# Performance work log

Hardware: AMD Instinct MI355X
Metric: run time of the kernel (lower is better)

Reference implementation:

```python
import jax, jax.numpy as jnp
import numpy as np

N_NODES = 50000
N_EDGES = 800000
D_IN = 128
D_HID = 512
D_OUT = 128


def setup_inputs() -> dict:
    key = jax.random.key(0)
    k1, k2, k3, k4, k5, k6 = jax.random.split(key, 6)
    input_matrix = jax.random.normal(k1, (N_NODES, D_IN), dtype=jnp.float32)
    adjacency_coo_matrix = jax.random.randint(k2, (2, N_EDGES), 0, N_NODES, dtype=jnp.int64)
    # fc net params (torch Linear: y = x @ W.T + b); store W already transposed [D_IN, D_HID]
    lim_fc = 1.0 / np.sqrt(D_IN)
    fc_w = jax.random.uniform(k3, (D_IN, D_HID), dtype=jnp.float32, minval=-lim_fc, maxval=lim_fc)
    fc_b = jax.random.uniform(k4, (D_HID,), dtype=jnp.float32, minval=-lim_fc, maxval=lim_fc)
    # xavier_uniform for [D_IN + D_HID, D_OUT]
    lim_w = np.sqrt(6.0 / (D_IN + D_HID + D_OUT))
    weights_matrix = jax.random.uniform(k5, (D_IN + D_HID, D_OUT), dtype=jnp.float32, minval=-lim_w, maxval=lim_w)
    return {
        "input_matrix": input_matrix,
        "fc_w": fc_w,
        "fc_b": fc_b,
        "weights_matrix": weights_matrix,
        "adjacency_coo_matrix": adjacency_coo_matrix,
    }


def reference(input_matrix, fc_w, fc_b, weights_matrix, adjacency_coo_matrix):
    edge_src, edge_trg = adjacency_coo_matrix[0], adjacency_coo_matrix[1]
    n_nodes = input_matrix.shape[0]
    # gather neighbor features: [E, D_IN]
    neighbors = input_matrix[edge_trg]
    # per-edge MLP + relu: [E, D_HID]
    neighbors_repr = jax.nn.relu(neighbors @ fc_w + fc_b)
    # scatter-max reduce into per-node slots; relu outputs are >= 0, and
    # empty segments map to 0 (matching torch_scatter zero-fill), so clamp at 0
    agg = jax.ops.segment_max(neighbors_repr, edge_src, num_segments=n_nodes)
    agg = jnp.maximum(agg, 0.0)
    concat = jnp.concatenate([input_matrix, agg], axis=1)  # [N, D_IN + D_HID]
    return concat @ weights_matrix  # [N, D_OUT]
```

## Files before the change

kernel.cpp:

```cpp
#include <hip/hip_runtime.h>
#include <hip/hip_bf16.h>

#define N_NODES 50000
#define N_EDGES 800000
#define D_IN 128
#define D_HID 512
#define D_OUT 128
#define CAT_DIM 640
#define CAP 64

typedef __attribute__((ext_vector_type(8))) short short8;
typedef __attribute__((ext_vector_type(4))) float floatx4;

__device__ __forceinline__ unsigned short f2bf(float f) {
    unsigned u = __float_as_uint(f);
    unsigned r = u + 0x7fffu + ((u >> 16) & 1u);
    return (unsigned short)(r >> 16);
}

__device__ __forceinline__ void cvt8(const float* __restrict__ src, unsigned short* o) {
    float4 v0 = *(const float4*)src;
    float4 v1 = *(const float4*)(src + 4);
    o[0] = f2bf(v0.x); o[1] = f2bf(v0.y); o[2] = f2bf(v0.z); o[3] = f2bf(v0.w);
    o[4] = f2bf(v1.x); o[5] = f2bf(v1.y); o[6] = f2bf(v1.z); o[7] = f2bf(v1.w);
}


#define NBKT 98
#define BKT_SHIFT 9
#define CAPB 12288
#define P1_CHUNK 4096
#define P1_BLOCKS 196


#define A_FCW_BLOCKS 256
#define A_W2_BLOCKS  320
#define A_BLOCKS (P1_BLOCKS + A_FCW_BLOCKS + A_W2_BLOCKS)

__global__ __launch_bounds__(256)
void prep_sort_kernel(const float* __restrict__ fcW, const float* __restrict__ Wm,
                      const int* __restrict__ adj,
                      unsigned short* __restrict__ fcwT,
                      unsigned short* __restrict__ WT,
                      int* __restrict__ bucket_cnt, uint2* __restrict__ staging) {
    int b = blockIdx.x, tid = threadIdx.x;
    if (b < P1_BLOCKS) {
        __shared__ uint2 les[P1_CHUNK];
        __shared__ int cnt[NBKT];
        __shared__ int woff[NBKT];
        for (int i = tid; i < NBKT; i += 256) cnt[i] = 0;
        int v = adj[2 * (tid & 63) + 1];
        int s = (__ballot(v != 0) == 0ULL) ? 2 : 1;
        __syncthreads();
        int e0 = b * P1_CHUNK;
        int ne = N_EDGES - e0; if (ne > P1_CHUNK) ne = P1_CHUNK;
        for (int j = tid; j < ne; j += 256) {
            int e = e0 + j;
            int src, trg;
            if (s == 2) { src = adj[2 * (size_t)e]; trg = adj[2 * ((size_t)N_EDGES + e)]; }
            else        { src = adj[e];             trg = adj[N_EDGES + e]; }
            les[j] = make_uint2((unsigned)src, (unsigned)trg);
            atomicAdd(&cnt[src >> BKT_SHIFT], 1);
        }
        __syncthreads();
        for (int i = tid; i < NBKT; i += 256)
            woff[i] = atomicAdd(&bucket_cnt[i], cnt[i]);
        __syncthreads();
        for (int j = tid; j < ne; j += 256) {
            uint2 et = les[j];
            int bk = (int)(et.x >> BKT_SHIFT);
            int pos = atomicAdd(&woff[bk], 1);
            if (pos < CAPB) staging[(size_t)bk * CAPB + pos] = et;
        }
        return;
    }
    b -= P1_BLOCKS;
    if (b < A_FCW_BLOCKS) {
        int idx = b * 256 + tid;
        int k = idx >> 9;
        int n = idx & (D_HID - 1);
        fcwT[n * D_IN + k] = f2bf(fcW[idx]);
        return;
    }
    b -= A_FCW_BLOCKS;
    {
        int idx = b * 256 + tid;
        int k = idx >> 7;
        int n = idx & (D_OUT - 1);
        WT[n * CAT_DIM + k] = f2bf(Wm[idx]);
    }
}


#define GEMM_MT      782
#define GEMM1_TILES (GEMM_MT * 4)
#define GPAD 8
#define SM_BYTES ((64 + 128) * (64 + GPAD) * 2)

__global__ __launch_bounds__(256)
void mid_kernel(const int* __restrict__ bucket_cnt, const uint2* __restrict__ staging,
                int* __restrict__ deg, int* __restrict__ edge_list,
                const float* __restrict__ X,
                const unsigned short* __restrict__ fcwT,
                const float* __restrict__ fcb,
                unsigned short* __restrict__ F) {
    __shared__ char smem[SM_BYTES];
    int tid = threadIdx.x;
    if (blockIdx.x < NBKT) {
        int* ldeg = (int*)smem;
        int bk = blockIdx.x;
        for (int i = tid; i < 512; i += 256) ldeg[i] = 0;
        __syncthreads();
        int n = bucket_cnt[bk]; if (n > CAPB) n = CAPB;
        int base = bk << BKT_SHIFT;
        const uint2* st = staging + (size_t)bk * CAPB;
        for (int i = tid; i < n; i += 256) {
            uint2 et = st[i];
            int p = atomicAdd(&ldeg[(int)et.x - base], 1);
            if (p < CAP) edge_list[(size_t)et.x * CAP + p] = (int)et.y;
        }
        __syncthreads();
        for (int i = tid; i < 512; i += 256) {
            int src = base + i;
            if (src < N_NODES) deg[src] = ldeg[i];
        }
        return;
    }
    typedef unsigned short RowA[64 + GPAD];
    RowA* As = (RowA*)smem;
    RowA* Bs = (RowA*)(smem + 64 * (64 + GPAD) * 2);
    int lane = tid & 63, w = tid >> 6;
    int tile = blockIdx.x - NBKT;
    int bm = (tile >> 2) * 64, bn = (tile & 3) * 128;
    int wm = (w >> 1) * 32, wn = (w & 1) * 64;
    int q = lane >> 4, l16 = lane & 15;
    floatx4 acc[2][4] = {};
    int ra = tid >> 2;
    int ca = (tid & 3) * 8;
    int rb = tid >> 1;
    int cb = (tid & 1) * 8;

    for (int k0 = 0; k0 < D_IN; k0 += 64) {
        {
            int gr = bm + ra;
            #pragma unroll
            for (int p = 0; p < 2; ++p) {
                unsigned short o[8] = {0, 0, 0, 0, 0, 0, 0, 0};
                if (gr < N_NODES) cvt8(X + (size_t)gr * D_IN + k0 + ca + p * 32, o);
                *(uint4*)(&As[ra][ca + p * 32]) = *(const uint4*)o;
            }
        }
        {
            const unsigned short* bp = fcwT + (size_t)(bn + rb) * D_IN + k0 + cb;
            #pragma unroll
            for (int p = 0; p < 4; ++p)
                *(uint4*)(&Bs[rb][cb + p * 16]) = *(const uint4*)(bp + p * 16);
        }
        __syncthreads();
        #pragma unroll
        for (int ks = 0; ks < 2; ++ks) {
            short8 af[2], bf[4];
            #pragma unroll
            for (int mi = 0; mi < 2; ++mi)
                af[mi] = *(const short8*)(&As[wm + mi * 16 + l16][ks * 32 + q * 8]);
            #pragma unroll
            for (int ni = 0; ni < 4; ++ni)
                bf[ni] = *(const short8*)(&Bs[wn + ni * 16 + l16][ks * 32 + q * 8]);
            #pragma unroll
            for (int mi = 0; mi < 2; ++mi)
                #pragma unroll
                for (int ni = 0; ni < 4; ++ni)
                    acc[mi][ni] = __builtin_amdgcn_mfma_f32_16x16x32_bf16(af[mi], bf[ni], acc[mi][ni], 0, 0, 0);
        }
        __syncthreads();
    }

    #pragma unroll
    for (int mi = 0; mi < 2; ++mi)
        #pragma unroll
        for (int ni = 0; ni < 4; ++ni)
            #pragma unroll
            for (int r = 0; r < 4; ++r) {
                int row = bm + wm + mi * 16 + q * 4 + r;
                int col = bn + wn + ni * 16 + l16;
                if (row < N_NODES) {
                    float v = fmaxf(acc[mi][ni][r] + fcb[col], 0.0f);
                    F[(size_t)row * D_HID + col] = f2bf(v);
                }
            }
}


__device__ __forceinline__ void fmax_bf16x8(float* acc, const uint4& p) {
    const unsigned* a = (const unsigned*)&p;
    #pragma unroll
    for (int j = 0; j < 4; ++j) {
        unsigned u = a[j];
        acc[2 * j]     = fmaxf(acc[2 * j],     __uint_as_float(u << 16));
        acc[2 * j + 1] = fmaxf(acc[2 * j + 1], __uint_as_float(u & 0xffff0000u));
    }
}

__global__ __launch_bounds__(256)
void aggregate_kernel(const unsigned short* __restrict__ F,
                      const int* __restrict__ deg,
                      const int* __restrict__ edge_list,
                      unsigned short* __restrict__ agg) {
    int gw = (blockIdx.x * 256 + threadIdx.x) >> 6;
    if (gw >= N_NODES) return;
    int lane = threadIdx.x & 63;
    int d = deg[gw];
    d = d < CAP ? d : CAP;
    const int* el = edge_list + gw * CAP;
    float acc[8] = {0.f, 0.f, 0.f, 0.f, 0.f, 0.f, 0.f, 0.f};
    int i = 0;
    for (; i + 2 <= d; i += 2) {
        int t0 = el[i], t1 = el[i + 1];
        uint4 p0 = *(const uint4*)(F + (size_t)t0 * D_HID + lane * 8);
        uint4 p1 = *(const uint4*)(F + (size_t)t1 * D_HID + lane * 8);
        fmax_bf16x8(acc, p0);
        fmax_bf16x8(acc, p1);
    }
    if (i < d) {
        uint4 p0 = *(const uint4*)(F + (size_t)el[i] * D_HID + lane * 8);
        fmax_bf16x8(acc, p0);
    }
    unsigned out[4];
    #pragma unroll
    for (int j = 0; j < 4; ++j) {
        unsigned lo = __float_as_uint(acc[2 * j]) >> 16;
        unsigned hi = __float_as_uint(acc[2 * j + 1]) & 0xffff0000u;
        out[j] = lo | hi;
    }
    *(uint4*)(agg + (size_t)gw * D_HID + lane * 8) = *(uint4*)out;
}


__global__ __launch_bounds__(256)
void gemm2_kernel(const float* __restrict__ X,
                  const unsigned short* __restrict__ agg,
                  const unsigned short* __restrict__ WT,
                  float* __restrict__ out) {
    __shared__ unsigned short As[64][64 + GPAD];
    __shared__ unsigned short Bs[128][64 + GPAD];
    int tid = threadIdx.x;
    int lane = tid & 63, w = tid >> 6;
    int wm = (w >> 1) * 32, wn = (w & 1) * 64;
    int q = lane >> 4, l16 = lane & 15;
    int bm = blockIdx.x * 64;
    floatx4 acc[2][4] = {};
    int ra = tid >> 2;
    int ca = (tid & 3) * 8;
    int rb = tid >> 1;
    int cb = (tid & 1) * 8;

    for (int k0 = 0; k0 < CAT_DIM; k0 += 64) {
        {
            int gr = bm + ra;
            #pragma unroll
            for (int p = 0; p < 2; ++p) {
                int col = k0 + ca + p * 32;
                unsigned short o[8] = {0, 0, 0, 0, 0, 0, 0, 0};
                if (gr < N_NODES) {
                    if (col < D_IN) cvt8(X + (size_t)gr * D_IN + col, o);
                    else *(uint4*)o = *(const uint4*)(agg + (size_t)gr * D_HID + (col - D_IN));
                }
                *(uint4*)(&As[ra][ca + p * 32]) = *(const uint4*)o;
            }
        }
        {
            const unsigned short* bp = WT + (size_t)rb * CAT_DIM + k0 + cb;
            #pragma unroll
            for (int p = 0; p < 4; ++p)
                *(uint4*)(&Bs[rb][cb + p * 16]) = *(const uint4*)(bp + p * 16);
        }
        __syncthreads();
        #pragma unroll
        for (int ks = 0; ks < 2; ++ks) {
            short8 af[2], bf[4];
            #pragma unroll
            for (int mi = 0; mi < 2; ++mi)
                af[mi] = *(const short8*)(&As[wm + mi * 16 + l16][ks * 32 + q * 8]);
            #pragma unroll
            for (int ni = 0; ni < 4; ++ni)
                bf[ni] = *(const short8*)(&Bs[wn + ni * 16 + l16][ks * 32 + q * 8]);
            #pragma unroll
            for (int mi = 0; mi < 2; ++mi)
                #pragma unroll
                for (int ni = 0; ni < 4; ++ni)
                    acc[mi][ni] = __builtin_amdgcn_mfma_f32_16x16x32_bf16(af[mi], bf[ni], acc[mi][ni], 0, 0, 0);
        }
        __syncthreads();
    }

    #pragma unroll
    for (int mi = 0; mi < 2; ++mi)
        #pragma unroll
        for (int ni = 0; ni < 4; ++ni)
            #pragma unroll
            for (int r = 0; r < 4; ++r) {
                int row = bm + wm + mi * 16 + q * 4 + r;
                int col = wn + ni * 16 + l16;
                if (row < N_NODES)
                    out[(size_t)row * D_OUT + col] = acc[mi][ni][r];
            }
}


extern "C" void kernel_launch(void* const* d_in, const int* in_sizes, int n_in,
                              void* d_out, int out_size, void* d_ws, size_t ws_size,
                              hipStream_t stream) {
    const float* X    = (const float*)d_in[0];
    const float* fc_w = (const float*)d_in[1];
    const float* fc_b = (const float*)d_in[2];
    const float* Wm   = (const float*)d_in[3];
    const int*   adj  = (const int*)d_in[4];
    float* outp = (float*)d_out;

    char* ws = (char*)d_ws;
    size_t off = 0;
    auto alloc = [&](size_t bytes) -> void* {
        void* p = ws + off;
        off = (off + bytes + 255) & ~(size_t)255;
        return p;
    };
    unsigned short* agg    = (unsigned short*)alloc((size_t)N_NODES * D_HID * 2);
    unsigned short* F      = (unsigned short*)alloc((size_t)N_NODES * D_HID * 2);
    unsigned short* fcwT   = (unsigned short*)alloc((size_t)D_HID * D_IN * 2);
    unsigned short* WT     = (unsigned short*)alloc((size_t)D_OUT * CAT_DIM * 2);
    int* deg       = (int*)alloc((size_t)N_NODES * 4);
    int* edge_list = (int*)alloc((size_t)N_NODES * CAP * 4);
    int* bucket_cnt = (int*)alloc((size_t)NBKT * 4);
    uint2* staging  = (uint2*)alloc((size_t)NBKT * CAPB * 8);

    hipMemsetAsync(bucket_cnt, 0, (size_t)NBKT * 4, stream);
    prep_sort_kernel<<<A_BLOCKS, 256, 0, stream>>>(fc_w, Wm, adj, fcwT, WT,
                                                   bucket_cnt, staging);
    mid_kernel<<<NBKT + GEMM1_TILES, 256, 0, stream>>>(bucket_cnt, staging,
                                                       deg, edge_list,
                                                       X, fcwT, fc_b, F);
    aggregate_kernel<<<(N_NODES * 64) / 256, 256, 0, stream>>>(F, deg, edge_list, agg);
    gemm2_kernel<<<GEMM_MT, 256, 0, stream>>>(X, agg, WT, outp);
}
```

Baseline: 278.8 us.

## Regroup kernels: overlap edge bucketing with GEMM1, split second sort pass

Moves the fc weight transpose into its own small kernel so GEMM1 can run in the same launch as the first edge-bucketing pass and the W transpose. GEMM1 now loads each 64-row X tile once with full K=128 and loops over the four 128-column output chunks, which removes the redundant X reloads and fp32-to-bf16 conversions. The second sort pass becomes a separate kernel with twice as many buckets (256 nodes each, smaller capacity). This trades one extra launch for better overlap and reuse, and the halved per-bucket capacity raises the risk of overflow under skewed degree distributions.

```diff
diff --git a/kernel.cpp b/kernel.cpp
--- a/kernel.cpp
+++ b/kernel.cpp
@@ -26,28 +26,44 @@
 }
 
 
-#define NBKT 98
-#define BKT_SHIFT 9
-#define CAPB 12288
+#define NBKT 196
+#define BKT_SHIFT 8
+#define CAPB 6144
 #define P1_CHUNK 4096
 #define P1_BLOCKS 196
 
 
-#define A_FCW_BLOCKS 256
-#define A_W2_BLOCKS  320
-#define A_BLOCKS (P1_BLOCKS + A_FCW_BLOCKS + A_W2_BLOCKS)
-
-__global__ __launch_bounds__(256)
-void prep_sort_kernel(const float* __restrict__ fcW, const float* __restrict__ Wm,
-                      const int* __restrict__ adj,
-                      unsigned short* __restrict__ fcwT,
-                      unsigned short* __restrict__ WT,
-                      int* __restrict__ bucket_cnt, uint2* __restrict__ staging) {
+#define K0_BLOCKS 256
+
+__global__ __launch_bounds__(256)
+void prep_fcw_kernel(const float* __restrict__ fcW, unsigned short* __restrict__ fcwT) {
+    int idx = blockIdx.x * 256 + threadIdx.x;
+    int k = idx >> 9;
+    int n = idx & (D_HID - 1);
+    fcwT[n * D_IN + k] = f2bf(fcW[idx]);
+}
+
+
+#define S1_G1_BLOCKS 782
+#define S1_WT_BLOCKS 320
+#define S1_BLOCKS (P1_BLOCKS + S1_G1_BLOCKS + S1_WT_BLOCKS)
+#define G1_PAD 8
+#define SM1_BYTES ((64 + 128) * (D_IN + G1_PAD) * 2)
+
+__global__ __launch_bounds__(256)
+void sort_gemm1_kernel(const int* __restrict__ adj,
+                       int* __restrict__ bucket_cnt, uint2* __restrict__ staging,
+                       const float* __restrict__ X,
+                       const unsigned short* __restrict__ fcwT,
+                       const float* __restrict__ fcb,
+                       unsigned short* __restrict__ F,
+                       const float* __restrict__ Wm, unsigned short* __restrict__ WT) {
+    __shared__ alignas(16) char smem[SM1_BYTES];
     int b = blockIdx.x, tid = threadIdx.x;
     if (b < P1_BLOCKS) {
-        __shared__ uint2 les[P1_CHUNK];
-        __shared__ int cnt[NBKT];
-        __shared__ int woff[NBKT];
+        uint2* les = (uint2*)smem;
+        int* cnt   = (int*)(smem + P1_CHUNK * 8);
+        int* woff  = cnt + NBKT;
         for (int i = tid; i < NBKT; i += 256) cnt[i] = 0;
         int v = adj[2 * (tid & 63) + 1];
         int s = (__ballot(v != 0) == 0ULL) ? 2 : 1;
@@ -75,14 +91,72 @@
         return;
     }
     b -= P1_BLOCKS;
-    if (b < A_FCW_BLOCKS) {
-        int idx = b * 256 + tid;
-        int k = idx >> 9;
-        int n = idx & (D_HID - 1);
-        fcwT[n * D_IN + k] = f2bf(fcW[idx]);
+    if (b < S1_G1_BLOCKS) {
+        typedef unsigned short RowG[D_IN + G1_PAD];
+        RowG* As = (RowG*)smem;
+        RowG* Bs = (RowG*)(smem + 64 * (D_IN + G1_PAD) * 2);
+        int lane = tid & 63, w = tid >> 6;
+        int bm = b * 64;
+        {
+            int r = tid >> 4;
+            int c = (tid & 15) * 8;
+            #pragma unroll
+            for (int p = 0; p < 4; ++p) {
+                int row = r + p * 16;
+                int gr = bm + row;
+                unsigned short o[8] = {0, 0, 0, 0, 0, 0, 0, 0};
+                if (gr < N_NODES) cvt8(X + (size_t)gr * D_IN + c, o);
+                *(uint4*)(&As[row][c]) = *(const uint4*)o;
+            }
+        }
+        int wm = (w >> 1) * 32, wn = (w & 1) * 64;
+        int q = lane >> 4, l16 = lane & 15;
+        for (int nc = 0; nc < 4; ++nc) {
+            {
+                int r = tid >> 4;
+                int c = (tid & 15) * 8;
+                #pragma unroll
+                for (int p = 0; p < 8; ++p) {
+                    int row = r + p * 16;
+                    *(uint4*)(&Bs[row][c]) =
+                        *(const uint4*)(fcwT + (size_t)(nc * 128 + row) * D_IN + c);
+                }
+            }
+            __syncthreads();
+            floatx4 acc[2][4] = {};
+            #pragma unroll
+            for (int ks = 0; ks < 4; ++ks) {
+                short8 af[2], bf[4];
+                #pragma unroll
+                for (int mi = 0; mi < 2; ++mi)
+                    af[mi] = *(const short8*)(&As[wm + mi * 16 + l16][ks * 32 + q * 8]);
+                #pragma unroll
+                for (int ni = 0; ni < 4; ++ni)
+                    bf[ni] = *(const short8*)(&Bs[wn + ni * 16 + l16][ks * 32 + q * 8]);
+                #pragma unroll
+                for (int mi = 0; mi < 2; ++mi)
+                    #pragma unroll
+                    for (int ni = 0; ni < 4; ++ni)
+                        acc[mi][ni] = __builtin_amdgcn_mfma_f32_16x16x32_bf16(af[mi], bf[ni], acc[mi][ni], 0, 0, 0);
+            }
+            #pragma unroll
+            for (int mi = 0; mi < 2; ++mi)
+                #pragma unroll
+                for (int ni = 0; ni < 4; ++ni)
+                    #pragma unroll
+                    for (int r = 0; r < 4; ++r) {
+                        int row = bm + wm + mi * 16 + q * 4 + r;
+                        int col = nc * 128 + wn + ni * 16 + l16;
+                        if (row < N_NODES) {
+                            float v = fmaxf(acc[mi][ni][r] + fcb[col], 0.0f);
+                            F[(size_t)row * D_HID + col] = f2bf(v);
+                        }
+                    }
+            __syncthreads();
+        }
         return;
     }
-    b -= A_FCW_BLOCKS;
+    b -= S1_G1_BLOCKS;
     {
         int idx = b * 256 + tid;
         int k = idx >> 7;
@@ -92,102 +166,24 @@
 }
 
 
-#define GEMM_MT      782
-#define GEMM1_TILES (GEMM_MT * 4)
-#define GPAD 8
-#define SM_BYTES ((64 + 128) * (64 + GPAD) * 2)
-
-__global__ __launch_bounds__(256)
-void mid_kernel(const int* __restrict__ bucket_cnt, const uint2* __restrict__ staging,
-                int* __restrict__ deg, int* __restrict__ edge_list,
-                const float* __restrict__ X,
-                const unsigned short* __restrict__ fcwT,
-                const float* __restrict__ fcb,
-                unsigned short* __restrict__ F) {
-    __shared__ char smem[SM_BYTES];
-    int tid = threadIdx.x;
-    if (blockIdx.x < NBKT) {
-        int* ldeg = (int*)smem;
-        int bk = blockIdx.x;
-        for (int i = tid; i < 512; i += 256) ldeg[i] = 0;
-        __syncthreads();
-        int n = bucket_cnt[bk]; if (n > CAPB) n = CAPB;
-        int base = bk << BKT_SHIFT;
-        const uint2* st = staging + (size_t)bk * CAPB;
-        for (int i = tid; i < n; i += 256) {
-            uint2 et = st[i];
-            int p = atomicAdd(&ldeg[(int)et.x - base], 1);
-            if (p < CAP) edge_list[(size_t)et.x * CAP + p] = (int)et.y;
-        }
-        __syncthreads();
-        for (int i = tid; i < 512; i += 256) {
-            int src = base + i;
-            if (src < N_NODES) deg[src] = ldeg[i];
-        }
-        return;
-    }
-    typedef unsigned short RowA[64 + GPAD];
-    RowA* As = (RowA*)smem;
-    RowA* Bs = (RowA*)(smem + 64 * (64 + GPAD) * 2);
-    int lane = tid & 63, w = tid >> 6;
-    int tile = blockIdx.x - NBKT;
-    int bm = (tile >> 2) * 64, bn = (tile & 3) * 128;
-    int wm = (w >> 1) * 32, wn = (w & 1) * 64;
-    int q = lane >> 4, l16 = lane & 15;
-    floatx4 acc[2][4] = {};
-    int ra = tid >> 2;
-    int ca = (tid & 3) * 8;
-    int rb = tid >> 1;
-    int cb = (tid & 1) * 8;
-
-    for (int k0 = 0; k0 < D_IN; k0 += 64) {
-        {
-            int gr = bm + ra;
-            #pragma unroll
-            for (int p = 0; p < 2; ++p) {
-                unsigned short o[8] = {0, 0, 0, 0, 0, 0, 0, 0};
-                if (gr < N_NODES) cvt8(X + (size_t)gr * D_IN + k0 + ca + p * 32, o);
-                *(uint4*)(&As[ra][ca + p * 32]) = *(const uint4*)o;
-            }
-        }
-        {
-            const unsigned short* bp = fcwT + (size_t)(bn + rb) * D_IN + k0 + cb;
-            #pragma unroll
-            for (int p = 0; p < 4; ++p)
-                *(uint4*)(&Bs[rb][cb + p * 16]) = *(const uint4*)(bp + p * 16);
-        }
-        __syncthreads();
-        #pragma unroll
-        for (int ks = 0; ks < 2; ++ks) {
-            short8 af[2], bf[4];
-            #pragma unroll
-            for (int mi = 0; mi < 2; ++mi)
-                af[mi] = *(const short8*)(&As[wm + mi * 16 + l16][ks * 32 + q * 8]);
-            #pragma unroll
-            for (int ni = 0; ni < 4; ++ni)
-                bf[ni] = *(const short8*)(&Bs[wn + ni * 16 + l16][ks * 32 + q * 8]);
-            #pragma unroll
-            for (int mi = 0; mi < 2; ++mi)
-                #pragma unroll
-                for (int ni = 0; ni < 4; ++ni)
-                    acc[mi][ni] = __builtin_amdgcn_mfma_f32_16x16x32_bf16(af[mi], bf[ni], acc[mi][ni], 0, 0, 0);
-        }
-        __syncthreads();
-    }
-
-    #pragma unroll
-    for (int mi = 0; mi < 2; ++mi)
-        #pragma unroll
-        for (int ni = 0; ni < 4; ++ni)
-            #pragma unroll
-            for (int r = 0; r < 4; ++r) {
-                int row = bm + wm + mi * 16 + q * 4 + r;
-                int col = bn + wn + ni * 16 + l16;
-                if (row < N_NODES) {
-                    float v = fmaxf(acc[mi][ni][r] + fcb[col], 0.0f);
-                    F[(size_t)row * D_HID + col] = f2bf(v);
-                }
-            }
+__global__ __launch_bounds__(256)
+void sort2_kernel(const int* __restrict__ bucket_cnt, const uint2* __restrict__ staging,
+                  int* __restrict__ deg, int* __restrict__ edge_list) {
+    __shared__ int ldeg[256];
+    int bk = blockIdx.x, tid = threadIdx.x;
+    ldeg[tid] = 0;
+    __syncthreads();
+    int n = bucket_cnt[bk]; if (n > CAPB) n = CAPB;
+    int base = bk << BKT_SHIFT;
+    const uint2* st = staging + (size_t)bk * CAPB;
+    for (int i = tid; i < n; i += 256) {
+        uint2 et = st[i];
+        int p = atomicAdd(&ldeg[(int)et.x - base], 1);
+        if (p < CAP) edge_list[(size_t)et.x * CAP + p] = (int)et.y;
+    }
+    __syncthreads();
+    int src = base + tid;
+    if (src < N_NODES) deg[src] = ldeg[tid];
 }
 
 
@@ -236,6 +232,9 @@
 }
 
 
+#define GPAD 8
+#define GEMM_MT 782
+
 __global__ __launch_bounds__(256)
 void gemm2_kernel(const float* __restrict__ X,
                   const unsigned short* __restrict__ agg,
@@ -334,11 +333,10 @@
     uint2* staging  = (uint2*)alloc((size_t)NBKT * CAPB * 8);
 
     hipMemsetAsync(bucket_cnt, 0, (size_t)NBKT * 4, stream);
-    prep_sort_kernel<<<A_BLOCKS, 256, 0, stream>>>(fc_w, Wm, adj, fcwT, WT,
-                                                   bucket_cnt, staging);
-    mid_kernel<<<NBKT + GEMM1_TILES, 256, 0, stream>>>(bucket_cnt, staging,
-                                                       deg, edge_list,
-                                                       X, fcwT, fc_b, F);
+    prep_fcw_kernel<<<K0_BLOCKS, 256, 0, stream>>>(fc_w, fcwT);
+    sort_gemm1_kernel<<<S1_BLOCKS, 256, 0, stream>>>(adj, bucket_cnt, staging,
+                                                     X, fcwT, fc_b, F, Wm, WT);
+    sort2_kernel<<<NBKT, 256, 0, stream>>>(bucket_cnt, staging, deg, edge_list);
     aggregate_kernel<<<(N_NODES * 64) / 256, 256, 0, stream>>>(F, deg, edge_list, agg);
     gemm2_kernel<<<GEMM_MT, 256, 0, stream>>>(X, agg, WT, outp);
 }
```

New measurement: 280.5 us. No clear change (+0.6%).
